# Optimization experiments

Measured on AMD Instinct MI355X. Metric: run time of the kernel, lower is better.

The kernel has to match this reference:

```python
import jax, jax.numpy as jnp
import numpy as np

B, N, BASE, H, W = 2, 262144, 10, 256, 256
EPS = 1e-9


def setup_inputs() -> dict:
    key = jax.random.key(0)
    kx, ky, kt, kp, kf = jax.random.split(key, 5)
    x = jax.random.uniform(kx, (B, N), minval=0.0, maxval=W - 1.0)
    y = jax.random.uniform(ky, (B, N), minval=0.0, maxval=H - 1.0)
    t = jax.random.uniform(kt, (B, N), minval=0.0, maxval=float(BASE))
    p = jax.random.randint(kp, (B, N), 0, 2).astype(jnp.float32)
    # events: (x, y, t_warp, t_stamp, polarity)
    events = jnp.stack([x, y, t, t, p], axis=-1)
    # flow per temporal bin, channels-last: [B, base, H, W, 2], in pixels/bin
    flow_maps = jax.random.normal(kf, (B, BASE, H, W, 2), dtype=jnp.float32) * 5.0
    return {"events": events, "flow_maps": flow_maps, "base": BASE}


def _bilinear_sample_flow(flow_maps, b_idx, zi, x, y):
    # flow_maps: [b, d, h, w, 2]; border-clamped bilinear sample at float (x, y)
    h, w = flow_maps.shape[2], flow_maps.shape[3]
    x0 = jnp.clip(jnp.floor(x).astype(jnp.int32), 0, w - 2)
    y0 = jnp.clip(jnp.floor(y).astype(jnp.int32), 0, h - 2)
    fx = jnp.clip(x - x0, 0.0, 1.0)
    fy = jnp.clip(y - y0, 0.0, 1.0)
    f00 = flow_maps[b_idx, zi, y0, x0]
    f01 = flow_maps[b_idx, zi, y0, x0 + 1]
    f10 = flow_maps[b_idx, zi, y0 + 1, x0]
    f11 = flow_maps[b_idx, zi, y0 + 1, x0 + 1]
    w00 = ((1 - fx) * (1 - fy))[..., None]
    w01 = (fx * (1 - fy))[..., None]
    w10 = ((1 - fx) * fy)[..., None]
    w11 = (fx * fy)[..., None]
    return w00 * f00 + w01 * f01 + w10 * f10 + w11 * f11  # [b, n, 2]


def _forward(events, flow_maps, base):
    b, n, _ = events.shape
    d, h, w = flow_maps.shape[1], flow_maps.shape[2], flow_maps.shape[3]
    R = base + 1  # number of warp references (all bin edges)
    x, y, t, ts, p = (events[..., i] for i in range(5))
    b_idx = jnp.broadcast_to(jnp.arange(b)[:, None], (b, n))
    zi = jnp.clip(jnp.floor(t).astype(jnp.int32), 0, d - 1)  # event's bin

    # linear 3d warp: sample flow at event location, warp to all R references
    flow = _bilinear_sample_flow(flow_maps, b_idx, zi, x, y)  # [b, n, 2]
    trefs = jnp.arange(R, dtype=events.dtype)
    dt = trefs[None, None, :] - t[..., None]                  # [b, n, R]
    wx = x[..., None] + dt * flow[..., 0:1]
    wy = y[..., None] + dt * flow[..., 1:2]

    # build_iwe: bilinear scatter-add into [b, 2(pol), R, h, w]
    p_idx = jnp.clip(p.astype(jnp.int32), 0, 1)
    chan = (b_idx * 2 + p_idx)[..., None] * R + jnp.arange(R)[None, None, :]
    flat_base = chan * (h * w)                                # [b, n, R]
    x0 = jnp.floor(wx).astype(jnp.int32)
    y0 = jnp.floor(wy).astype(jnp.int32)
    fx = wx - x0
    fy = wy - y0
    tv = jnp.broadcast_to(ts[..., None], wx.shape).ravel()
    iwe = jnp.zeros(b * 2 * R * h * w, dtype=events.dtype)
    iwt = jnp.zeros(b * 2 * R * h * w, dtype=events.dtype)
    corners = ((x0, y0, (1 - fx) * (1 - fy)),
               (x0 + 1, y0, fx * (1 - fy)),
               (x0, y0 + 1, (1 - fx) * fy),
               (x0 + 1, y0 + 1, fx * fy))
    for xi, yi, wc in corners:
        valid = (xi >= 0) & (xi < w) & (yi >= 0) & (yi < h)
        idx = jnp.where(valid, flat_base + yi * w + xi, 0).ravel()
        wv = jnp.where(valid, wc, 0.0).ravel()
        iwe = iwe.at[idx].add(wv)
        iwt = iwt.at[idx].add(wv * tv)
    iwe = iwe.reshape(b, 2, R, h, w)
    iwt = iwt.reshape(b, 2, R, h, w)

    # contrast-maximization loss on image of warped average timestamps
    iwat = iwt / (iwe + EPS)
    inside = (iwe.sum(1) > 0).astype(events.dtype).reshape(b, R, -1).sum(-1) + EPS
    loss = (iwat ** 2).sum(axis=(1, 3, 4))  # neg^2 + pos^2, summed over h*w
    return loss / inside  # [b, R]


def reference(events, flow_maps, base):
    return _forward(events, flow_maps, base)
```

## Files before the change

### kernel.cpp

```cpp
#include <hip/hip_runtime.h>

#define NB 2
#define NN 262144
#define ND 10
#define NR 11
#define HH 256
#define WW 256
#define HWSZ 65536
#define SROWS 8
#define NSTRIP 32
#define PLANE (SROWS * WW)
#define BINS_B (NR * NSTRIP)
#define NBIN (NB * BINS_B)
#define BINCAP (2u * NB * NN * NR)
#define EPSF 1e-9f

#define SC_E 2097152.0f
#define SC_T 524288.0f
#define ISC_E (1.0f / 2097152.0f)
#define ISC_T (1.0f / 524288.0f)


__device__ __forceinline__ unsigned classify(float ax, float ay, float dx, float dy, float rf)
{
    float wx = fmaf(rf, dx, ax);
    float wy = fmaf(rf, dy, ay);
    int xi = (int)floorf(wx);
    int yi = (int)floorf(wy);
    if (xi + 1 < 0 || xi >= WW || yi + 1 < 0 || yi >= HH) return 0xFFu;
    int rr = yi < 0 ? 0 : yi;
    unsigned s = (unsigned)(rr >> 3);
    unsigned str = (yi >= 0 && yi + 1 < HH && ((yi & 7) == 7)) ? 0x40u : 0u;
    return s | str;
}

__global__ __launch_bounds__(1024) void cm_prep(
    const float* __restrict__ events,
    const float* __restrict__ flow,
    float4* __restrict__ rec,
    float* __restrict__ tspol,
    unsigned* __restrict__ counts)
{
    __shared__ unsigned hist[BINS_B];
    for (int i = threadIdx.x; i < BINS_B; i += 1024) hist[i] = 0u;
    __syncthreads();

    int gid = blockIdx.x * 1024 + threadIdx.x;
    int b = gid >> 18;

    const float* e = events + (size_t)gid * 5;
    float x  = e[0];
    float y  = e[1];
    float t  = e[2];
    float ts = e[3];
    float p  = e[4];

    int zi = (int)floorf(t);
    zi = zi < 0 ? 0 : (zi > ND - 1 ? ND - 1 : zi);
    int x0 = (int)floorf(x);
    x0 = x0 < 0 ? 0 : (x0 > WW - 2 ? WW - 2 : x0);
    int y0 = (int)floorf(y);
    y0 = y0 < 0 ? 0 : (y0 > HH - 2 ? HH - 2 : y0);
    float fx = fminf(fmaxf(x - (float)x0, 0.0f), 1.0f);
    float fy = fminf(fmaxf(y - (float)y0, 0.0f), 1.0f);

    const float2* f2 = (const float2*)flow + ((size_t)b * ND + zi) * HWSZ;
    float2 f00 = f2[y0 * WW + x0];
    float2 f01 = f2[y0 * WW + x0 + 1];
    float2 f10 = f2[(y0 + 1) * WW + x0];
    float2 f11 = f2[(y0 + 1) * WW + x0 + 1];
    float w00 = (1.0f - fx) * (1.0f - fy);
    float w01 = fx * (1.0f - fy);
    float w10 = (1.0f - fx) * fy;
    float w11 = fx * fy;
    float dx = w00 * f00.x + w01 * f01.x + w10 * f10.x + w11 * f11.x;
    float dy = w00 * f00.y + w01 * f01.y + w10 * f10.y + w11 * f11.y;
    float ax = fmaf(-t, dx, x);
    float ay = fmaf(-t, dy, y);

    rec[gid] = make_float4(ax, ay, dx, dy);
    int pi = (p != 0.0f) ? 1 : 0;
    tspol[gid] = __int_as_float(__float_as_int(ts) | (pi << 31));

    #pragma unroll
    for (int r = 0; r < NR; ++r) {
        unsigned c = classify(ax, ay, dx, dy, (float)r);
        if (c != 0xFFu) {
            int bin = r * NSTRIP + (int)(c & 31u);
            atomicAdd(&hist[bin], 1u);
            if (c & 0x40u) atomicAdd(&hist[bin + 1], 1u);
        }
    }
    __syncthreads();
    for (int i = threadIdx.x; i < BINS_B; i += 1024) {
        unsigned c = hist[i];
        if (c) atomicAdd(&counts[b * BINS_B + i], c);
    }
}

__global__ __launch_bounds__(1024) void cm_prefix(
    const unsigned* __restrict__ counts,
    unsigned* __restrict__ starts,
    unsigned* __restrict__ cursors)
{
    __shared__ unsigned sa[1024];
    int tid = threadIdx.x;

    unsigned v = (tid < NBIN) ? counts[tid] : 0u;
    sa[tid] = v;
    __syncthreads();
    for (int off = 1; off < 1024; off <<= 1) {
        unsigned x = sa[tid];
        if (tid >= off) x += sa[tid - off];
        __syncthreads();
        sa[tid] = x;
        __syncthreads();
    }
    if (tid < NBIN) {
        unsigned ex = tid ? sa[tid - 1] : 0u;
        starts[tid] = ex;
        cursors[tid] = ex;
    }
    if (tid == 0) starts[NBIN] = sa[NBIN - 1];
}

__global__ __launch_bounds__(1024) void cm_fill(
    const float4* __restrict__ rec,
    const float* __restrict__ tspol,
    float* __restrict__ bins,
    unsigned* __restrict__ cursors)
{
    __shared__ unsigned char stash[2048 * NR];
    __shared__ unsigned cnt[BINS_B];
    __shared__ unsigned base[BINS_B];

    for (int i = threadIdx.x; i < BINS_B; i += 1024) cnt[i] = 0u;
    __syncthreads();

    int e0 = blockIdx.x * 2048;
    int b = e0 >> 18;

    float4 ea[2];
    float tp[2];
    #pragma unroll
    for (int k = 0; k < 2; ++k) {
        int el = e0 + k * 1024 + threadIdx.x;
        ea[k] = rec[el];
        tp[k] = tspol[el];
    }

    #pragma unroll
    for (int k = 0; k < 2; ++k) {
        int sl = (k * 1024 + threadIdx.x) * NR;
        for (int r = 0; r < NR; ++r) {
            unsigned c = classify(ea[k].x, ea[k].y, ea[k].z, ea[k].w, (float)r);
            stash[sl + r] = (unsigned char)c;
            if (c != 0xFFu) {
                int bin = r * NSTRIP + (int)(c & 31u);
                atomicAdd(&cnt[bin], 1u);
                if (c & 0x40u) atomicAdd(&cnt[bin + 1], 1u);
            }
        }
    }
    __syncthreads();
    for (int i = threadIdx.x; i < BINS_B; i += 1024) {
        unsigned c = cnt[i];
        base[i] = c ? atomicAdd(&cursors[b * BINS_B + i], c) : 0u;
    }
    __syncthreads();
    for (int i = threadIdx.x; i < BINS_B; i += 1024) cnt[i] = 0u;
    __syncthreads();

    #pragma unroll
    for (int k = 0; k < 2; ++k) {
        int sl = (k * 1024 + threadIdx.x) * NR;
        for (int r = 0; r < NR; ++r) {
            unsigned c = stash[sl + r];
            if (c != 0xFFu) {
                float rf = (float)r;
                float wx = fmaf(rf, ea[k].z, ea[k].x);
                float wy = fmaf(rf, ea[k].w, ea[k].y);
                int bin = r * NSTRIP + (int)(c & 31u);
                unsigned rank = atomicAdd(&cnt[bin], 1u);
                size_t o = (size_t)(base[bin] + rank) * 3;
                bins[o + 0] = wx;
                bins[o + 1] = wy;
                bins[o + 2] = tp[k];
                if (c & 0x40u) {
                    unsigned rank2 = atomicAdd(&cnt[bin + 1], 1u);
                    size_t o2 = (size_t)(base[bin + 1] + rank2) * 3;
                    bins[o2 + 0] = wx;
                    bins[o2 + 1] = wy;
                    bins[o2 + 2] = tp[k];
                }
            }
        }
    }
}

__global__ __launch_bounds__(1024) void cm_scan(
    const float* __restrict__ bins,
    const unsigned* __restrict__ starts,
    float* __restrict__ accum)
{
    __shared__ unsigned long long acc8[2 * PLANE];
    __shared__ float red[32];

    int blk = blockIdx.x;
    int b  = blk / BINS_B;
    int rm = blk - b * BINS_B;
    int r  = rm >> 5;
    int s  = rm & 31;
    int ty0 = s * SROWS;

    for (int i = threadIdx.x; i < 2 * PLANE; i += 1024) acc8[i] = 0ull;
    __syncthreads();

    unsigned lo = starts[blk];
    unsigned hi = starts[blk + 1];

    for (unsigned bse = lo; bse < hi; bse += 4096) {
        float wxv[4], wyv[4], ets[4];
        bool  val[4];
        #pragma unroll
        for (int k = 0; k < 4; ++k) {
            unsigned i = bse + (unsigned)(k * 1024) + threadIdx.x;
            val[k] = i < hi;
            unsigned j = val[k] ? i : (hi - 1);
            size_t o = (size_t)j * 3;
            wxv[k] = bins[o + 0];
            wyv[k] = bins[o + 1];
            ets[k] = bins[o + 2];
        }
        __builtin_amdgcn_sched_barrier(0);
        #pragma unroll
        for (int k = 0; k < 4; ++k) {
            if (!val[k]) continue;
            float wxk = wxv[k], wyk = wyv[k], tpv = ets[k];
            int pi = (int)((unsigned)__float_as_int(tpv) >> 31);
            float tsv = fabsf(tpv);
            float fwx = floorf(wxk);
            float fwy = floorf(wyk);
            int xi = (int)fwx;
            int yi = (int)fwy;
            float axf = wxk - fwx;
            float ayf = wyk - fwy;
            unsigned long long* ap = acc8 + pi * PLANE;
            float c00 = (1.0f - axf) * (1.0f - ayf);
            float c01 = axf * (1.0f - ayf);
            float c10 = (1.0f - axf) * ayf;
            float c11 = axf * ayf;
            #define CM_CORNER(XI, YI, WV)                                          \
                if ((XI) >= 0 && (XI) < WW && (YI) >= ty0 && (YI) < ty0 + SROWS) { \
                    int liq = ((YI) - ty0) * WW + (XI);                            \
                    unsigned pe = __float2uint_rn((WV) * SC_E);                    \
                    unsigned pt = __float2uint_rn((WV) * tsv * SC_T);              \
                    atomicAdd(&ap[liq],                                            \
                              ((unsigned long long)pt << 32) | (unsigned long long)pe); \
                }
            CM_CORNER(xi,     yi,     c00)
            CM_CORNER(xi + 1, yi,     c01)
            CM_CORNER(xi,     yi + 1, c10)
            CM_CORNER(xi + 1, yi + 1, c11)
            #undef CM_CORNER
        }
    }
    __syncthreads();

    float ss = 0.0f, ins = 0.0f;
    for (int i = threadIdx.x; i < PLANE; i += 1024) {
        unsigned long long v0 = acc8[i];
        unsigned long long v1 = acc8[PLANE + i];
        unsigned e0i = (unsigned)(v0 & 0xFFFFFFFFull);
        unsigned e1i = (unsigned)(v1 & 0xFFFFFFFFull);
        float e0 = (float)e0i * ISC_E;
        float t0 = (float)(unsigned)(v0 >> 32) * ISC_T;
        float e1 = (float)e1i * ISC_E;
        float t1 = (float)(unsigned)(v1 >> 32) * ISC_T;
        float a0 = t0 / (e0 + EPSF);
        float a1 = t1 / (e1 + EPSF);
        ss += a0 * a0 + a1 * a1;
        ins += ((e0i | e1i) != 0u) ? 1.0f : 0.0f;
    }
    #pragma unroll
    for (int off = 32; off > 0; off >>= 1) {
        ss  += __shfl_down(ss, off, 64);
        ins += __shfl_down(ins, off, 64);
    }
    int lane = threadIdx.x & 63;
    int wv = threadIdx.x >> 6;
    if (lane == 0) { red[2 * wv] = ss; red[2 * wv + 1] = ins; }
    __syncthreads();
    if (threadIdx.x == 0) {
        float tss = 0.0f, tin = 0.0f;
        #pragma unroll
        for (int w = 0; w < 16; ++w) { tss += red[2 * w]; tin += red[2 * w + 1]; }
        int br = b * NR + r;
        atomicAdd(&accum[br * 2],     tss);
        atomicAdd(&accum[br * 2 + 1], tin);
    }
}

__global__ void cm_final(const float* __restrict__ accum, float* __restrict__ out)
{
    int i = threadIdx.x;
    if (i < NB * NR) {
        out[i] = accum[i * 2] / (accum[i * 2 + 1] + EPSF);
    }
}

extern "C" void kernel_launch(void* const* d_in, const int* in_sizes, int n_in,
                              void* d_out, int out_size, void* d_ws, size_t ws_size,
                              hipStream_t stream) {
    const float* events = (const float*)d_in[0];
    const float* flow   = (const float*)d_in[1];

    char* ws = (char*)d_ws;
    size_t off = 0;
    float* bins = (float*)(ws + off);          off += (size_t)BINCAP * 3 * 4;
    float4* rec = (float4*)(ws + off);         off += (size_t)NB * NN * sizeof(float4);
    float* tspol = (float*)(ws + off);         off += (size_t)NB * NN * sizeof(float);
    unsigned* counts = (unsigned*)(ws + off);  off += NBIN * 4;
    float* accum = (float*)(ws + off);         off += 256;
    unsigned* starts = (unsigned*)(ws + off);  off += (NBIN + 1) * 4 + 60; off &= ~63ull;
    unsigned* cursors = (unsigned*)(ws + off); off += NBIN * 4;

    hipMemsetAsync(counts, 0, NBIN * 4 + 256, stream);

    cm_prep<<<NB * NN / 1024, 1024, 0, stream>>>(events, flow, rec, tspol, counts);

    cm_prefix<<<1, 1024, 0, stream>>>(counts, starts, cursors);

    cm_fill<<<NB * NN / 2048, 1024, 0, stream>>>(rec, tspol, bins, cursors);

    cm_scan<<<NBIN, 1024, 0, stream>>>(bins, starts, accum);

    cm_final<<<1, 64, 0, stream>>>(accum, (float*)d_out);
}
```

Measured before the change: 144.5 us.

## Pack binned warped events into 64-bit fixed-point entries with vectorized loads

The fill kernel now encodes each warped event as one 64-bit word: x and strip-relative y in fixed point, a 20-bit quantized timestamp and a polarity bit. This replaces three separate floats. The scan kernel reads four entries per thread through two 16-byte loads and decodes them, which cuts bin traffic from 12 to 8 bytes per entry and widens the loads. The cost is quantization of the coordinates and timestamp, plus decode arithmetic, and loads can start on an odd entry so the first one is handled separately.

```diff
diff --git a/kernel.cpp b/kernel.cpp
--- a/kernel.cpp
+++ b/kernel.cpp
@@ -127,7 +127,7 @@
 __global__ __launch_bounds__(1024) void cm_fill(
     const float4* __restrict__ rec,
     const float* __restrict__ tspol,
-    float* __restrict__ bins,
+    unsigned long long* __restrict__ bins,
     unsigned* __restrict__ cursors)
 {
     __shared__ unsigned char stash[2048 * NR];
@@ -174,24 +174,33 @@
     #pragma unroll
     for (int k = 0; k < 2; ++k) {
         int sl = (k * 1024 + threadIdx.x) * NR;
+        float tpv = tp[k];
+        unsigned pol = (unsigned)__float_as_int(tpv) >> 31;
+        float tsv = fabsf(tpv);
+        unsigned et = __float2uint_rn(tsv * 65536.0f);
+        unsigned long long hdr = ((unsigned long long)et << 43) |
+                                 ((unsigned long long)pol << 63);
         for (int r = 0; r < NR; ++r) {
             unsigned c = stash[sl + r];
             if (c != 0xFFu) {
                 float rf = (float)r;
                 float wx = fmaf(rf, ea[k].z, ea[k].x);
                 float wy = fmaf(rf, ea[k].w, ea[k].y);
-                int bin = r * NSTRIP + (int)(c & 31u);
+                int sid = (int)(c & 31u);
+                float ty0f = (float)(sid * SROWS);
+                unsigned ex = __float2uint_rn((wx + 1.0f) * 32768.0f);
+                unsigned ey = __float2uint_rn((wy - ty0f + 1.0f) * 32768.0f);
+                unsigned long long ent = hdr | (unsigned long long)ex |
+                                         ((unsigned long long)ey << 24);
+                int bin = r * NSTRIP + sid;
                 unsigned rank = atomicAdd(&cnt[bin], 1u);
-                size_t o = (size_t)(base[bin] + rank) * 3;
-                bins[o + 0] = wx;
-                bins[o + 1] = wy;
-                bins[o + 2] = tp[k];
+                bins[base[bin] + rank] = ent;
                 if (c & 0x40u) {
+                    unsigned ey2 = __float2uint_rn((wy - ty0f - (float)SROWS + 1.0f) * 32768.0f);
+                    unsigned long long ent2 = hdr | (unsigned long long)ex |
+                                              ((unsigned long long)ey2 << 24);
                     unsigned rank2 = atomicAdd(&cnt[bin + 1], 1u);
-                    size_t o2 = (size_t)(base[bin + 1] + rank2) * 3;
-                    bins[o2 + 0] = wx;
-                    bins[o2 + 1] = wy;
-                    bins[o2 + 2] = tp[k];
+                    bins[base[bin + 1] + rank2] = ent2;
                 }
             }
         }
@@ -199,7 +208,7 @@
 }
 
 __global__ __launch_bounds__(1024) void cm_scan(
-    const float* __restrict__ bins,
+    const unsigned long long* __restrict__ bins,
     const unsigned* __restrict__ starts,
     float* __restrict__ accum)
 {
@@ -210,8 +219,6 @@
     int b  = blk / BINS_B;
     int rm = blk - b * BINS_B;
     int r  = rm >> 5;
-    int s  = rm & 31;
-    int ty0 = s * SROWS;
 
     for (int i = threadIdx.x; i < 2 * PLANE; i += 1024) acc8[i] = 0ull;
     __syncthreads();
@@ -219,51 +226,53 @@
     unsigned lo = starts[blk];
     unsigned hi = starts[blk + 1];
 
-    for (unsigned bse = lo; bse < hi; bse += 4096) {
-        float wxv[4], wyv[4], ets[4];
-        bool  val[4];
-        #pragma unroll
-        for (int k = 0; k < 4; ++k) {
-            unsigned i = bse + (unsigned)(k * 1024) + threadIdx.x;
-            val[k] = i < hi;
-            unsigned j = val[k] ? i : (hi - 1);
-            size_t o = (size_t)j * 3;
-            wxv[k] = bins[o + 0];
-            wyv[k] = bins[o + 1];
-            ets[k] = bins[o + 2];
-        }
+    auto process = [&](unsigned long long e) {
+        float wx  = (float)(unsigned)(e & 0xFFFFFFu) * (1.0f / 32768.0f) - 1.0f;
+        float wyr = (float)(unsigned)((e >> 24) & 0x7FFFFu) * (1.0f / 32768.0f) - 1.0f;
+        float tsv = (float)(unsigned)((e >> 43) & 0xFFFFFu) * (1.0f / 65536.0f);
+        int pi = (int)(e >> 63);
+        float fwx = floorf(wx);
+        float fwy = floorf(wyr);
+        int xi = (int)fwx;
+        int yi = (int)fwy;
+        float axf = wx - fwx;
+        float ayf = wyr - fwy;
+        unsigned long long* ap = acc8 + pi * PLANE;
+        float c00 = (1.0f - axf) * (1.0f - ayf);
+        float c01 = axf * (1.0f - ayf);
+        float c10 = (1.0f - axf) * ayf;
+        float c11 = axf * ayf;
+        #define CM_CORNER(XI, YI, WV)                                          \
+            if ((XI) >= 0 && (XI) < WW && (YI) >= 0 && (YI) < SROWS) {         \
+                int liq = (YI) * WW + (XI);                                    \
+                unsigned pe = __float2uint_rn((WV) * SC_E);                    \
+                unsigned pt = __float2uint_rn((WV) * tsv * SC_T);              \
+                atomicAdd(&ap[liq],                                            \
+                          ((unsigned long long)pt << 32) | (unsigned long long)pe); \
+            }
+        CM_CORNER(xi,     yi,     c00)
+        CM_CORNER(xi + 1, yi,     c01)
+        CM_CORNER(xi,     yi + 1, c10)
+        CM_CORNER(xi + 1, yi + 1, c11)
+        #undef CM_CORNER
+    };
+
+    unsigned lo2 = lo + (lo & 1u);
+    if ((lo & 1u) && threadIdx.x == 0 && lo < hi) process(bins[lo]);
+
+    const uint4* bv = (const uint4*)bins;
+    for (unsigned bse = lo2 + 4u * threadIdx.x; bse < hi; bse += 4096u) {
+        uint4 A = bv[bse >> 1];
+        uint4 B = bv[(bse >> 1) + 1];
         __builtin_amdgcn_sched_barrier(0);
-        #pragma unroll
-        for (int k = 0; k < 4; ++k) {
-            if (!val[k]) continue;
-            float wxk = wxv[k], wyk = wyv[k], tpv = ets[k];
-            int pi = (int)((unsigned)__float_as_int(tpv) >> 31);
-            float tsv = fabsf(tpv);
-            float fwx = floorf(wxk);
-            float fwy = floorf(wyk);
-            int xi = (int)fwx;
-            int yi = (int)fwy;
-            float axf = wxk - fwx;
-            float ayf = wyk - fwy;
-            unsigned long long* ap = acc8 + pi * PLANE;
-            float c00 = (1.0f - axf) * (1.0f - ayf);
-            float c01 = axf * (1.0f - ayf);
-            float c10 = (1.0f - axf) * ayf;
-            float c11 = axf * ayf;
-            #define CM_CORNER(XI, YI, WV)                                          \
-                if ((XI) >= 0 && (XI) < WW && (YI) >= ty0 && (YI) < ty0 + SROWS) { \
-                    int liq = ((YI) - ty0) * WW + (XI);                            \
-                    unsigned pe = __float2uint_rn((WV) * SC_E);                    \
-                    unsigned pt = __float2uint_rn((WV) * tsv * SC_T);              \
-                    atomicAdd(&ap[liq],                                            \
-                              ((unsigned long long)pt << 32) | (unsigned long long)pe); \
-                }
-            CM_CORNER(xi,     yi,     c00)
-            CM_CORNER(xi + 1, yi,     c01)
-            CM_CORNER(xi,     yi + 1, c10)
-            CM_CORNER(xi + 1, yi + 1, c11)
-            #undef CM_CORNER
-        }
+        unsigned long long e0 = (unsigned long long)A.x | ((unsigned long long)A.y << 32);
+        unsigned long long e1 = (unsigned long long)A.z | ((unsigned long long)A.w << 32);
+        unsigned long long e2 = (unsigned long long)B.x | ((unsigned long long)B.y << 32);
+        unsigned long long e3 = (unsigned long long)B.z | ((unsigned long long)B.w << 32);
+        process(e0);
+        if (bse + 1 < hi) process(e1);
+        if (bse + 2 < hi) process(e2);
+        if (bse + 3 < hi) process(e3);
     }
     __syncthreads();
 
@@ -317,7 +326,8 @@
 
     char* ws = (char*)d_ws;
     size_t off = 0;
-    float* bins = (float*)(ws + off);          off += (size_t)BINCAP * 3 * 4;
+    unsigned long long* bins = (unsigned long long*)(ws + off);
+    off += (size_t)BINCAP * 8;
     float4* rec = (float4*)(ws + off);         off += (size_t)NB * NN * sizeof(float4);
     float* tspol = (float*)(ws + off);         off += (size_t)NB * NN * sizeof(float);
     unsigned* counts = (unsigned*)(ws + off);  off += NBIN * 4;
```

Result: faster. 139.9 us (-3.2%).
